# Kernel tuning notes

Hardware: AMD Instinct MI355X
Metric: run time of the kernel (lower is better)

The kernel has to match this reference:

```python
import jax, jax.numpy as jnp
from jax import lax
import numpy as np

EPS = 1e-3  # Keras BatchNormalization default epsilon

def cond_conv(x, experts, rw, rb):
    # x: [B,H,W,Cin]; experts: [E,kh,kw,Cin,Cout]
    pooled = jnp.mean(x, axis=(1, 2))                       # [B,Cin]
    route = jax.nn.sigmoid(pooled @ rw + rb)                # [B,E]
    kernels = jnp.einsum('be,ehwio->bhwio', route, experts) # per-example kernel
    def conv1(xi, ki):
        return lax.conv_general_dilated(
            xi[None], ki, window_strides=(1, 1), padding='SAME',
            dimension_numbers=('NHWC', 'HWIO', 'NHWC'))[0]
    return jax.vmap(conv1)(x, kernels)

def bn_inf(x, gamma, beta, mean, var):
    inv = gamma * lax.rsqrt(var + EPS)
    return x * inv + (beta - mean * inv)

def maxpool2(x):
    return lax.reduce_window(x, -jnp.inf, lax.max,
                             (1, 2, 2, 1), (1, 2, 2, 1), 'SAME')

def se_block(x, w1, w2):
    s = jnp.mean(x, axis=(1, 2))          # [B,C]
    s = jax.nn.relu(s @ w1)
    s = jax.nn.sigmoid(s @ w2)
    return x * s[:, None, None, :]

def setup_inputs() -> dict:
    key = jax.random.key(0)
    ks = jax.random.split(key, 12)
    d = {
        'x': jax.random.normal(ks[0], (64, 128, 128, 6), jnp.float32),
        'experts1': jax.random.normal(ks[1], (3, 3, 3, 6, 32), jnp.float32) * 0.1,
        'route1_w': jax.random.normal(ks[2], (6, 3), jnp.float32) * 0.1,
        'route1_b': jnp.zeros((3,), jnp.float32),
        'bn1_gamma': jnp.ones((32,), jnp.float32), 'bn1_beta': jnp.zeros((32,), jnp.float32),
        'bn1_mean': jnp.zeros((32,), jnp.float32), 'bn1_var': jnp.ones((32,), jnp.float32),
        'se1_w1': jax.random.normal(ks[3], (32, 2), jnp.float32) * 0.1,
        'se1_w2': jax.random.normal(ks[4], (2, 32), jnp.float32) * 0.1,
        'experts2': jax.random.normal(ks[5], (3, 3, 3, 32, 64), jnp.float32) * 0.05,
        'route2_w': jax.random.normal(ks[6], (32, 3), jnp.float32) * 0.1,
        'route2_b': jnp.zeros((3,), jnp.float32),
        'bn2_gamma': jnp.ones((64,), jnp.float32), 'bn2_beta': jnp.zeros((64,), jnp.float32),
        'bn2_mean': jnp.zeros((64,), jnp.float32), 'bn2_var': jnp.ones((64,), jnp.float32),
        'se2_w1': jax.random.normal(ks[7], (64, 4), jnp.float32) * 0.1,
        'se2_w2': jax.random.normal(ks[8], (4, 64), jnp.float32) * 0.1,
        'experts3': jax.random.normal(ks[9], (3, 3, 3, 64, 128), jnp.float32) * 0.05,
        'route3_w': jax.random.normal(ks[10], (64, 3), jnp.float32) * 0.1,
        'route3_b': jnp.zeros((3,), jnp.float32),
        'bn3_gamma': jnp.ones((128,), jnp.float32), 'bn3_beta': jnp.zeros((128,), jnp.float32),
        'bn3_mean': jnp.zeros((128,), jnp.float32), 'bn3_var': jnp.ones((128,), jnp.float32),
    }
    return d

def reference(x, experts1, route1_w, route1_b, bn1_gamma, bn1_beta, bn1_mean, bn1_var,
              se1_w1, se1_w2, experts2, route2_w, route2_b, bn2_gamma, bn2_beta,
              bn2_mean, bn2_var, se2_w1, se2_w2, experts3, route3_w, route3_b,
              bn3_gamma, bn3_beta, bn3_mean, bn3_var):
    h = cond_conv(x, experts1, route1_w, route1_b)
    h = jax.nn.relu(bn_inf(h, bn1_gamma, bn1_beta, bn1_mean, bn1_var))
    h = maxpool2(h)                       # [B,64,64,32]
    h = se_block(h, se1_w1, se1_w2)
    h = cond_conv(h, experts2, route2_w, route2_b)
    h = jax.nn.relu(bn_inf(h, bn2_gamma, bn2_beta, bn2_mean, bn2_var))
    h = maxpool2(h)                       # [B,32,32,64]
    h = se_block(h, se2_w1, se2_w2)
    h = cond_conv(h, experts3, route3_w, route3_b)
    h = bn_inf(h, bn3_gamma, bn3_beta, bn3_mean, bn3_var)
    return jnp.mean(h, axis=(1, 2))       # [B,128]
```

## Files before the change

kernel.cpp:

```cpp
#include <hip/hip_runtime.h>

#define EPSBN 1e-3f

typedef unsigned short ushort_t;
typedef __attribute__((ext_vector_type(8))) short bf8;
typedef __attribute__((ext_vector_type(4))) float f4;

__device__ __forceinline__ float sigmoidf_(float z) {
  return 1.0f / (1.0f + expf(-z));
}

__device__ __forceinline__ ushort_t f2bf(float x) {
  union { float f; unsigned u; } v; v.f = x;
  unsigned r = (v.u + 0x7fffu + ((v.u >> 16) & 1u)) >> 16;
  return (ushort_t)r;
}

__global__ void k_mean_x(const float* __restrict__ x, float* __restrict__ part) {
  const int b = blockIdx.x >> 2;
  const int q = blockIdx.x & 3;
  const int tid = threadIdx.x;
  float acc[6] = {0.f, 0.f, 0.f, 0.f, 0.f, 0.f};
  const float* xb = x + (size_t)b * 98304 + (size_t)q * 24576;
  for (int p = 0; p < 4; ++p) {
    const float* base = xb + (size_t)p * 6144 + (size_t)tid * 24;
#pragma unroll
    for (int k = 0; k < 6; ++k) {
      const float4 v = *(const float4*)(base + k * 4);
      acc[(4 * k + 0) % 6] += v.x;
      acc[(4 * k + 1) % 6] += v.y;
      acc[(4 * k + 2) % 6] += v.z;
      acc[(4 * k + 3) % 6] += v.w;
    }
  }
#pragma unroll
  for (int c = 0; c < 6; ++c)
    for (int off = 32; off > 0; off >>= 1) acc[c] += __shfl_down(acc[c], off, 64);
  __shared__ float red[4][6];
  const int lane = tid & 63, w = tid >> 6;
  if (lane == 0) {
#pragma unroll
    for (int c = 0; c < 6; ++c) red[w][c] = acc[c];
  }
  __syncthreads();
  if (tid < 6) {
    part[blockIdx.x * 6 + tid] = red[0][tid] + red[1][tid] + red[2][tid] + red[3][tid];
  }
}

__global__ __launch_bounds__(256)
void k_conv1(const float* __restrict__ x, const float* __restrict__ meanx_part,
             const float* __restrict__ experts1,
             const float* __restrict__ rw, const float* __restrict__ rbias,
             const float* __restrict__ gamma, const float* __restrict__ beta,
             const float* __restrict__ bnmean, const float* __restrict__ bnvar,
             ushort_t* __restrict__ p1b, float* __restrict__ part_m1) {
  const int bid = blockIdx.x;
  const int b = bid >> 3;
  const int tyi = (bid >> 1) & 3;
  const int txi = bid & 1;
  __shared__ __align__(16) ushort_t patch[34 * 68 * 8];
  __shared__ float route_s[3];
  __shared__ float mred[4][32];
  const int tid = threadIdx.x;
  const float* xb = x + (size_t)b * (128 * 128 * 6);

  if (tid < 3) {
    float z = rbias[tid];
    for (int c = 0; c < 6; ++c) {
      const float s = meanx_part[(b * 4 + 0) * 6 + c] + meanx_part[(b * 4 + 1) * 6 + c] +
                      meanx_part[(b * 4 + 2) * 6 + c] + meanx_part[(b * 4 + 3) * 6 + c];
      z += (s * (1.0f / 16384.0f)) * rw[c * 3 + tid];
    }
    route_s[tid] = sigmoidf_(z);
  }

  for (int v = tid; v < 34 * 68; v += 256) {
    const int ry = v / 68, p = v - ry * 68;
    const int gy = tyi * 32 - 1 + ry, gx = txi * 64 - 1 + p;
    uint4 u = make_uint4(0u, 0u, 0u, 0u);
    if (((unsigned)gy < 128u) && ((unsigned)gx < 128u)) {
      const float* s = xb + ((size_t)(gy * 128 + gx)) * 6;
      const float2 a0 = *(const float2*)s;
      const float2 a1 = *(const float2*)(s + 2);
      const float2 a2 = *(const float2*)(s + 4);
      u.x = (unsigned)f2bf(a0.x) | ((unsigned)f2bf(a0.y) << 16);
      u.y = (unsigned)f2bf(a1.x) | ((unsigned)f2bf(a1.y) << 16);
      u.z = (unsigned)f2bf(a2.x) | ((unsigned)f2bf(a2.y) << 16);
      u.w = 0u;
    }
    *(uint4*)(patch + (size_t)v * 8) = u;
  }
  __syncthreads();

  const int w = tid >> 6;
  const int lane = tid & 63;
  const int lx = lane & 15, lg = lane >> 4;

  const float r0 = route_s[0], r1 = route_s[1], r2 = route_s[2];
  const int co0 = lx, co1 = 16 + lx;
  const float inv0 = gamma[co0] * rsqrtf(bnvar[co0] + EPSBN);
  const float bias0 = beta[co0] - bnmean[co0] * inv0;
  const float inv1 = gamma[co1] * rsqrtf(bnvar[co1] + EPSBN);
  const float bias1 = beta[co1] - bnmean[co1] * inv1;

  bf8 Bf[3][2];
#pragma unroll
  for (int ky = 0; ky < 3; ++ky) {
#pragma unroll
    for (int nt = 0; nt < 2; ++nt) {
      const int co = nt * 16 + lx;
      const float inv = nt ? inv1 : inv0;
#pragma unroll
      for (int j = 0; j < 8; ++j) {
        float val = 0.f;
        if (j < 6 && lg < 3) {
          const int idx = ((ky * 3 + lg) * 6 + j) * 32 + co;
          val = (r0 * experts1[idx] + r1 * experts1[1728 + idx] +
                 r2 * experts1[3456 + idx]) * inv;
        }
        Bf[ky][nt][j] = (short)f2bf(val);
      }
    }
  }

  float msum0 = 0.f, msum1 = 0.f;

#pragma unroll
  for (int xt = 0; xt < 4; ++xt) {
    bf8 Af[10];
#pragma unroll
    for (int r = 0; r < 10; ++r)
      Af[r] = *(const bf8*)(patch + ((size_t)(w * 8 + r) * 68 + xt * 16 + lx + lg) * 8);
#pragma unroll
    for (int rp = 0; rp < 4; ++rp) {
      const int prow = tyi * 16 + w * 4 + rp;
      f4 acc0[2], acc1[2];
#pragma unroll
      for (int nt = 0; nt < 2; ++nt) {
        acc0[nt] = (f4){0.f, 0.f, 0.f, 0.f};
        acc1[nt] = (f4){0.f, 0.f, 0.f, 0.f};
      }
#pragma unroll
      for (int ky = 0; ky < 3; ++ky) {
#pragma unroll
        for (int nt = 0; nt < 2; ++nt) {
          acc0[nt] = __builtin_amdgcn_mfma_f32_16x16x32_bf16(Af[rp * 2 + ky], Bf[ky][nt], acc0[nt], 0, 0, 0);
          acc1[nt] = __builtin_amdgcn_mfma_f32_16x16x32_bf16(Af[rp * 2 + ky + 1], Bf[ky][nt], acc1[nt], 0, 0, 0);
        }
      }
#pragma unroll
      for (int nt = 0; nt < 2; ++nt) {
        const float bias = nt ? bias1 : bias0;
        const int co = nt * 16 + lx;
#pragma unroll
        for (int q = 0; q < 2; ++q) {
          const float m0 = fmaxf(acc0[nt][2 * q] + bias, 0.f);
          const float m1 = fmaxf(acc0[nt][2 * q + 1] + bias, 0.f);
          const float m2 = fmaxf(acc1[nt][2 * q] + bias, 0.f);
          const float m3 = fmaxf(acc1[nt][2 * q + 1] + bias, 0.f);
          const float mx = fmaxf(fmaxf(m0, m1), fmaxf(m2, m3));
          if (nt) msum1 += mx; else msum0 += mx;
          const int pcol = txi * 32 + xt * 8 + lg * 2 + q;
          p1b[(((size_t)b * 64 + prow) * 64 + pcol) * 32 + co] = f2bf(mx);
        }
      }
    }
  }

  msum0 += __shfl_xor(msum0, 16, 64);
  msum0 += __shfl_xor(msum0, 32, 64);
  msum1 += __shfl_xor(msum1, 16, 64);
  msum1 += __shfl_xor(msum1, 32, 64);
  if (lg == 0) {
    mred[w][lx] = msum0;
    mred[w][16 + lx] = msum1;
  }
  __syncthreads();
  if (tid < 32) {
    part_m1[(size_t)bid * 32 + tid] =
        mred[0][tid] + mred[1][tid] + mred[2][tid] + mred[3][tid];
  }
}

__global__ void k_buildk2(const float* __restrict__ part_m1,
                          const float* __restrict__ experts2,
                          const float* __restrict__ rw, const float* __restrict__ rb,
                          const float* __restrict__ w1, const float* __restrict__ w2,
                          const float* __restrict__ gamma, const float* __restrict__ var,
                          ushort_t* __restrict__ k2pb) {
  const int b = blockIdx.x / 3;
  const int seg = blockIdx.x - b * 3;
  const int tid = threadIdx.x;
  __shared__ float m1[32], h[2], s1[32], route[3];
  if (tid < 32) {
    float s = 0.f;
#pragma unroll
    for (int k = 0; k < 8; ++k) s += part_m1[(size_t)(b * 8 + k) * 32 + tid];
    m1[tid] = s * (1.0f / 4096.0f);
  }
  __syncthreads();
  if (tid < 2) {
    float z = 0.f;
    for (int c = 0; c < 32; ++c) z += m1[c] * w1[c * 2 + tid];
    h[tid] = fmaxf(z, 0.f);
  }
  __syncthreads();
  if (tid < 32) s1[tid] = sigmoidf_(h[0] * w2[tid] + h[1] * w2[32 + tid]);
  __syncthreads();
  if (tid < 3) {
    float z = rb[tid];
    for (int c = 0; c < 32; ++c) z += m1[c] * s1[c] * rw[c * 3 + tid];
    route[tid] = sigmoidf_(z);
  }
  __syncthreads();
  const float r0 = route[0], r1 = route[1], r2 = route[2];
  const int t_lo = seg * 6144, t_hi = t_lo + 6144;
  for (int t = t_lo + tid; t < t_hi; t += 256) {
    const int co = t & 63;
    const int ci = (t >> 6) & 31;
    const int tap = t >> 11;
    const float inv = gamma[co] * rsqrtf(var[co] + EPSBN);
    const float v = r0 * experts2[t] + r1 * experts2[18432 + t] + r2 * experts2[2 * 18432 + t];
    k2pb[(size_t)b * 18432 + ((size_t)tap * 64 + co) * 32 + ci] = f2bf(v * s1[ci] * inv);
  }
}

__global__ __launch_bounds__(256)
void k_conv2(const ushort_t* __restrict__ p1b, const ushort_t* __restrict__ k2pb,
             const float* __restrict__ gamma, const float* __restrict__ beta,
             const float* __restrict__ bnmean, const float* __restrict__ bnvar,
             float* __restrict__ part_s3) {
  const int bi = blockIdx.x;
  const int b = bi >> 5;
  const int tile = (bi >> 1) & 15;
  const int cog = bi & 1;
  const int ty = tile >> 2, tx = tile & 3;
  __shared__ __align__(16) short smem[24480];
  short* As = smem;
  short* Bs = smem + 12960;
  const int tid = threadIdx.x;

  const ushort_t* pb = p1b + (size_t)b * 131072;
  for (int v = tid; v < 1296; v += 256) {
    const int cell = v >> 2, part = v & 3;
    const int ly = cell / 18, lx2 = cell - ly * 18;
    const int gy = ty * 16 - 1 + ly, gx = tx * 16 - 1 + lx2;
    uint4 d = make_uint4(0u, 0u, 0u, 0u);
    if (((unsigned)gy < 64u) && ((unsigned)gx < 64u))
      d = *(const uint4*)(pb + (((size_t)gy << 6) + gx) * 32 + part * 8);
    *(uint4*)(As + (ly * 18 + lx2) * 40 + part * 8) = d;
  }
  for (int v = tid; v < 1152; v += 256) {
    const int r = v >> 2, part = v & 3;
    const int t = r >> 5, n = r & 31;
    const uint4 d = *(const uint4*)(k2pb + (size_t)b * 18432 +
                                    ((size_t)(t * 64 + cog * 32 + n)) * 32 + part * 8);
    *(uint4*)(Bs + r * 40 + part * 8) = d;
  }
  __syncthreads();

  const int w = tid >> 6;
  const int lane = tid & 63;
  const int lx = lane & 15, lg = lane >> 4;

  f4 acc[4][2];
#pragma unroll
  for (int mt = 0; mt < 4; ++mt)
#pragma unroll
    for (int nt = 0; nt < 2; ++nt)
      acc[mt][nt] = (f4){0.f, 0.f, 0.f, 0.f};

#pragma unroll
  for (int kx = 0; kx < 3; ++kx) {
    bf8 Af[6];
#pragma unroll
    for (int r = 0; r < 6; ++r)
      Af[r] = *(const bf8*)(As + ((4 * w + r) * 18 + lx + kx) * 40 + (lg << 3));
#pragma unroll
    for (int ky = 0; ky < 3; ++ky) {
      const int t = ky * 3 + kx;
      const bf8 Bf0 = *(const bf8*)(Bs + ((t << 5) + lx) * 40 + (lg << 3));
      const bf8 Bf1 = *(const bf8*)(Bs + ((t << 5) + 16 + lx) * 40 + (lg << 3));
#pragma unroll
      for (int mt = 0; mt < 4; ++mt) {
        acc[mt][0] = __builtin_amdgcn_mfma_f32_16x16x32_bf16(Af[ky + mt], Bf0, acc[mt][0], 0, 0, 0);
        acc[mt][1] = __builtin_amdgcn_mfma_f32_16x16x32_bf16(Af[ky + mt], Bf1, acc[mt][1], 0, 0, 0);
      }
    }
  }

  float inv[2], bias[2];
#pragma unroll
  for (int nt = 0; nt < 2; ++nt) {
    const int co = cog * 32 + nt * 16 + lx;
    inv[nt] = gamma[co] * rsqrtf(bnvar[co] + EPSBN);
    bias[nt] = beta[co] - bnmean[co] * inv[nt];
  }
  float agg[2][9];
#pragma unroll
  for (int nt = 0; nt < 2; ++nt)
#pragma unroll
    for (int a = 0; a < 9; ++a) agg[nt][a] = 0.f;

#pragma unroll
  for (int half = 0; half < 2; ++half) {
    const int prow = ty * 8 + 2 * w + half;
    const bool rT = (prow == 0), rB = (prow == 31);
#pragma unroll
    for (int q = 0; q < 2; ++q) {
      const int pcol = tx * 8 + 2 * lg + q;
      const bool cL = (pcol == 0), cR = (pcol == 31);
#pragma unroll
      for (int nt = 0; nt < 2; ++nt) {
        const float m0 = fmaxf(acc[2 * half][nt][2 * q] + bias[nt], 0.f);
        const float m1 = fmaxf(acc[2 * half][nt][2 * q + 1] + bias[nt], 0.f);
        const float m2 = fmaxf(acc[2 * half + 1][nt][2 * q] + bias[nt], 0.f);
        const float m3 = fmaxf(acc[2 * half + 1][nt][2 * q + 1] + bias[nt], 0.f);
        const float mx = fmaxf(fmaxf(m0, m1), fmaxf(m2, m3));
        agg[nt][0] += mx;
        if (rT) agg[nt][1] += mx;
        if (rB) agg[nt][2] += mx;
        if (cL) agg[nt][3] += mx;
        if (cR) agg[nt][4] += mx;
        if (rT && cL) agg[nt][5] += mx;
        if (rT && cR) agg[nt][6] += mx;
        if (rB && cL) agg[nt][7] += mx;
        if (rB && cR) agg[nt][8] += mx;
      }
    }
  }

#pragma unroll
  for (int nt = 0; nt < 2; ++nt)
#pragma unroll
    for (int a = 0; a < 9; ++a) {
      float v = agg[nt][a];
      v += __shfl_xor(v, 16, 64);
      v += __shfl_xor(v, 32, 64);
      agg[nt][a] = v;
    }
  __syncthreads();
  float* sred = (float*)smem;
  if (lg == 0) {
#pragma unroll
    for (int nt = 0; nt < 2; ++nt)
#pragma unroll
      for (int a = 0; a < 9; ++a)
        sred[((w * 2 + nt) * 16 + lx) * 9 + a] = agg[nt][a];
  }
  __syncthreads();
  for (int v = tid; v < 288; v += 256) {
    const int a = v >> 5;
    const int colocal = v & 31;
    const int nt = colocal >> 4, lxx = colocal & 15;
    float s = 0.f;
#pragma unroll
    for (int ww = 0; ww < 4; ++ww) s += sred[((ww * 2 + nt) * 16 + lxx) * 9 + a];
    part_s3[(size_t)bi * 288 + v] = s;
  }
}

__global__ __launch_bounds__(512)
void k_final(const float* __restrict__ part_s3, const float* __restrict__ experts3,
             const float* __restrict__ rw, const float* __restrict__ rb,
             const float* __restrict__ w1, const float* __restrict__ w2,
             const float* __restrict__ gamma, const float* __restrict__ beta,
             const float* __restrict__ bnmean, const float* __restrict__ bnvar,
             float* __restrict__ out) {
  const int b = blockIdx.x;
  const int tid = threadIdx.x;
  __shared__ float AG[9][64], Sp[9][64], m2[64], h[4], s2[64], route[3], redf[4][128];

  for (int v = tid; v < 576; v += 512) {
    const int a = v >> 6, ci = v & 63;
    const int cg = ci >> 5, colocal = ci & 31;
    float s = 0.f;
#pragma unroll
    for (int tile = 0; tile < 16; ++tile)
      s += part_s3[(size_t)((b * 16 + tile) * 2 + cg) * 288 + a * 32 + colocal];
    AG[a][ci] = s;
  }
  __syncthreads();
  if (tid < 64) m2[tid] = AG[0][tid] * (1.0f / 1024.0f);
  __syncthreads();
  if (tid < 4) {
    float z = 0.f;
    for (int c = 0; c < 64; ++c) z += m2[c] * w1[c * 4 + tid];
    h[tid] = fmaxf(z, 0.f);
  }
  __syncthreads();
  if (tid < 64) {
    float z = 0.f;
#pragma unroll
    for (int j = 0; j < 4; ++j) z += h[j] * w2[j * 64 + tid];
    s2[tid] = sigmoidf_(z);
  }
  __syncthreads();
  if (tid < 3) {
    float z = rb[tid];
    for (int c = 0; c < 64; ++c) z += m2[c] * s2[c] * rw[c * 3 + tid];
    route[tid] = sigmoidf_(z);
  }
  __syncthreads();
  for (int v = tid; v < 576; v += 512) {
    const int tap = v >> 6, ci = v & 63;
    const int ky = tap / 3, kx = tap - 3 * ky;
    const float T = AG[0][ci];
    const float A = (ky == 0) ? AG[2][ci] : ((ky == 2) ? AG[1][ci] : 0.f);
    const float B = (kx == 0) ? AG[4][ci] : ((kx == 2) ? AG[3][ci] : 0.f);
    float AB = 0.f;
    if (ky == 0 && kx == 0) AB = AG[8][ci];
    else if (ky == 0 && kx == 2) AB = AG[7][ci];
    else if (ky == 2 && kx == 0) AB = AG[6][ci];
    else if (ky == 2 && kx == 2) AB = AG[5][ci];
    Sp[tap][ci] = (T - A - B + AB) * s2[ci];
  }
  __syncthreads();

  const int co = tid & 127;
  const int quarter = tid >> 7;
  const int tap_lo = (quarter == 0) ? 0 : (2 * quarter + 1);
  const int tap_hi = tap_lo + ((quarter == 0) ? 3 : 2);
  float acc = 0.f;
#pragma unroll
  for (int e = 0; e < 3; ++e) {
    float m = 0.f;
    for (int tap = tap_lo; tap < tap_hi; ++tap) {
      const float* E = experts3 + ((size_t)(e * 9 + tap) * 64) * 128 + co;
#pragma unroll 16
      for (int ci = 0; ci < 64; ++ci) m = fmaf(E[(size_t)ci * 128], Sp[tap][ci], m);
    }
    acc += route[e] * m;
  }
  redf[quarter][co] = acc;
  __syncthreads();
  if (tid < 128) {
    const float total = redf[0][tid] + redf[1][tid] + redf[2][tid] + redf[3][tid];
    const float inv = gamma[tid] * rsqrtf(bnvar[tid] + EPSBN);
    out[(size_t)b * 128 + tid] = total * (1.0f / 1024.0f) * inv + (beta[tid] - bnmean[tid] * inv);
  }
}

extern "C" void kernel_launch(void* const* d_in, const int* in_sizes, int n_in,
                              void* d_out, int out_size, void* d_ws, size_t ws_size,
                              hipStream_t stream) {
  const float* x        = (const float*)d_in[0];
  const float* experts1 = (const float*)d_in[1];
  const float* rw1      = (const float*)d_in[2];
  const float* rb1      = (const float*)d_in[3];
  const float* g1  = (const float*)d_in[4];
  const float* be1 = (const float*)d_in[5];
  const float* mu1 = (const float*)d_in[6];
  const float* va1 = (const float*)d_in[7];
  const float* sw1a = (const float*)d_in[8];
  const float* sw1b = (const float*)d_in[9];
  const float* experts2 = (const float*)d_in[10];
  const float* rw2 = (const float*)d_in[11];
  const float* rb2 = (const float*)d_in[12];
  const float* g2  = (const float*)d_in[13];
  const float* be2 = (const float*)d_in[14];
  const float* mu2 = (const float*)d_in[15];
  const float* va2 = (const float*)d_in[16];
  const float* sw2a = (const float*)d_in[17];
  const float* sw2b = (const float*)d_in[18];
  const float* experts3 = (const float*)d_in[19];
  const float* rw3 = (const float*)d_in[20];
  const float* rb3 = (const float*)d_in[21];
  const float* g3  = (const float*)d_in[22];
  const float* be3 = (const float*)d_in[23];
  const float* mu3 = (const float*)d_in[24];
  const float* va3 = (const float*)d_in[25];
  float* out = (float*)d_out;
  float* ws = (float*)d_ws;

  float* meanx_part = ws;
  float* part_m1    = ws + 1536;
  ushort_t* k2pb    = (ushort_t*)(ws + 17920);
  float* part_s3    = ws + 607744;
  ushort_t* p1b     = (ushort_t*)(ws + 1197568);

  hipLaunchKernelGGL(k_mean_x, dim3(256), dim3(256), 0, stream, x, meanx_part);
  hipLaunchKernelGGL(k_conv1, dim3(512), dim3(256), 0, stream,
                     x, meanx_part, experts1, rw1, rb1, g1, be1, mu1, va1, p1b, part_m1);
  hipLaunchKernelGGL(k_buildk2, dim3(192), dim3(256), 0, stream,
                     part_m1, experts2, rw2, rb2, sw1a, sw1b, g2, va2, k2pb);
  hipLaunchKernelGGL(k_conv2, dim3(2048), dim3(256), 0, stream,
                     p1b, k2pb, g2, be2, mu2, va2, part_s3);
  hipLaunchKernelGGL(k_final, dim3(64), dim3(512), 0, stream,
                     part_s3, experts3, rw3, rb3, sw2a, sw2b, g3, be3, mu3, va3, out);
}
```

Before: 191.8 us.

## Pre-convert input to padded bf16, merge conv2 channel groups, fuse expert loop

The mean-reduction kernel now also writes the input as padded 8-channel bf16, so conv1's halo loads become single 16-byte reads without per-pixel conversion. conv2 has each block loop over both 32-channel output groups, reusing the loaded input patch and halving the grid. The final kernel computes all three expert sums in one pass over ci. The trade-off is an extra bf16 workspace write and read, and less parallelism in conv2.

After: 195.7 us. 2.1% more time.

```diff
diff --git a/kernel.cpp b/kernel.cpp
--- a/kernel.cpp
+++ b/kernel.cpp
@@ -16,40 +16,56 @@
   return (ushort_t)r;
 }
 
-__global__ void k_mean_x(const float* __restrict__ x, float* __restrict__ part) {
-  const int b = blockIdx.x >> 2;
-  const int q = blockIdx.x & 3;
+__global__ __launch_bounds__(256)
+void k_prep(const float* __restrict__ x, float* __restrict__ part,
+            ushort_t* __restrict__ xb16) {
+  const int bid = blockIdx.x;
   const int tid = threadIdx.x;
+  __shared__ __align__(16) float raw[3072];
+  __shared__ float red[4][6];
   float acc[6] = {0.f, 0.f, 0.f, 0.f, 0.f, 0.f};
-  const float* xb = x + (size_t)b * 98304 + (size_t)q * 24576;
-  for (int p = 0; p < 4; ++p) {
-    const float* base = xb + (size_t)p * 6144 + (size_t)tid * 24;
-#pragma unroll
-    for (int k = 0; k < 6; ++k) {
-      const float4 v = *(const float4*)(base + k * 4);
-      acc[(4 * k + 0) % 6] += v.x;
-      acc[(4 * k + 1) % 6] += v.y;
-      acc[(4 * k + 2) % 6] += v.z;
-      acc[(4 * k + 3) % 6] += v.w;
-    }
-  }
+  const size_t pixbase = (size_t)(bid >> 3) * 16384 + (size_t)(bid & 7) * 2048;
+  const float* xq = x + pixbase * 6;
+  ushort_t* oq = xb16 + pixbase * 8;
+  for (int ph = 0; ph < 4; ++ph) {
+    const float4* src = (const float4*)(xq + (size_t)ph * 3072);
+#pragma unroll
+    for (int i = 0; i < 3; ++i)
+      *(float4*)(raw + (i * 256 + tid) * 4) = src[i * 256 + tid];
+    __syncthreads();
+#pragma unroll
+    for (int h = 0; h < 2; ++h) {
+      const int pix = h * 256 + tid;
+      const float* r = raw + pix * 6;
+      const float2 p01 = *(const float2*)(r);
+      const float2 p23 = *(const float2*)(r + 2);
+      const float2 p45 = *(const float2*)(r + 4);
+      acc[0] += p01.x; acc[1] += p01.y; acc[2] += p23.x;
+      acc[3] += p23.y; acc[4] += p45.x; acc[5] += p45.y;
+      uint4 u;
+      u.x = (unsigned)f2bf(p01.x) | ((unsigned)f2bf(p01.y) << 16);
+      u.y = (unsigned)f2bf(p23.x) | ((unsigned)f2bf(p23.y) << 16);
+      u.z = (unsigned)f2bf(p45.x) | ((unsigned)f2bf(p45.y) << 16);
+      u.w = 0u;
+      *(uint4*)(oq + ((size_t)ph * 512 + pix) * 8) = u;
+    }
+    __syncthreads();
+  }
+  const int lane = tid & 63, w = tid >> 6;
 #pragma unroll
   for (int c = 0; c < 6; ++c)
     for (int off = 32; off > 0; off >>= 1) acc[c] += __shfl_down(acc[c], off, 64);
-  __shared__ float red[4][6];
-  const int lane = tid & 63, w = tid >> 6;
   if (lane == 0) {
 #pragma unroll
     for (int c = 0; c < 6; ++c) red[w][c] = acc[c];
   }
   __syncthreads();
-  if (tid < 6) {
-    part[blockIdx.x * 6 + tid] = red[0][tid] + red[1][tid] + red[2][tid] + red[3][tid];
-  }
+  if (tid < 6)
+    part[bid * 6 + tid] = red[0][tid] + red[1][tid] + red[2][tid] + red[3][tid];
 }
 
 __global__ __launch_bounds__(256)
-void k_conv1(const float* __restrict__ x, const float* __restrict__ meanx_part,
+void k_conv1(const ushort_t* __restrict__ xb16, const float* __restrict__ meanx_part,
              const float* __restrict__ experts1,
              const float* __restrict__ rw, const float* __restrict__ rbias,
              const float* __restrict__ gamma, const float* __restrict__ beta,
@@ -63,13 +79,14 @@
   __shared__ float route_s[3];
   __shared__ float mred[4][32];
   const int tid = threadIdx.x;
-  const float* xb = x + (size_t)b * (128 * 128 * 6);
+  const ushort_t* xb = xb16 + (size_t)b * 131072;
 
   if (tid < 3) {
     float z = rbias[tid];
     for (int c = 0; c < 6; ++c) {
-      const float s = meanx_part[(b * 4 + 0) * 6 + c] + meanx_part[(b * 4 + 1) * 6 + c] +
-                      meanx_part[(b * 4 + 2) * 6 + c] + meanx_part[(b * 4 + 3) * 6 + c];
+      float s = 0.f;
+#pragma unroll
+      for (int k = 0; k < 8; ++k) s += meanx_part[(b * 8 + k) * 6 + c];
       z += (s * (1.0f / 16384.0f)) * rw[c * 3 + tid];
     }
     route_s[tid] = sigmoidf_(z);
@@ -79,16 +96,8 @@
     const int ry = v / 68, p = v - ry * 68;
     const int gy = tyi * 32 - 1 + ry, gx = txi * 64 - 1 + p;
     uint4 u = make_uint4(0u, 0u, 0u, 0u);
-    if (((unsigned)gy < 128u) && ((unsigned)gx < 128u)) {
-      const float* s = xb + ((size_t)(gy * 128 + gx)) * 6;
-      const float2 a0 = *(const float2*)s;
-      const float2 a1 = *(const float2*)(s + 2);
-      const float2 a2 = *(const float2*)(s + 4);
-      u.x = (unsigned)f2bf(a0.x) | ((unsigned)f2bf(a0.y) << 16);
-      u.y = (unsigned)f2bf(a1.x) | ((unsigned)f2bf(a1.y) << 16);
-      u.z = (unsigned)f2bf(a2.x) | ((unsigned)f2bf(a2.y) << 16);
-      u.w = 0u;
-    }
+    if (((unsigned)gy < 128u) && ((unsigned)gx < 128u))
+      u = *(const uint4*)(xb + ((size_t)(gy * 128 + gx)) * 8);
     *(uint4*)(patch + (size_t)v * 8) = u;
   }
   __syncthreads();
@@ -232,11 +241,10 @@
              const float* __restrict__ bnmean, const float* __restrict__ bnvar,
              float* __restrict__ part_s3) {
   const int bi = blockIdx.x;
-  const int b = bi >> 5;
-  const int tile = (bi >> 1) & 15;
-  const int cog = bi & 1;
+  const int b = bi >> 4;
+  const int tile = bi & 15;
   const int ty = tile >> 2, tx = tile & 3;
-  __shared__ __align__(16) short smem[24480];
+  __shared__ __align__(16) short smem[12960 + 11520];
   short* As = smem;
   short* Bs = smem + 12960;
   const int tid = threadIdx.x;
@@ -251,113 +259,118 @@
       d = *(const uint4*)(pb + (((size_t)gy << 6) + gx) * 32 + part * 8);
     *(uint4*)(As + (ly * 18 + lx2) * 40 + part * 8) = d;
   }
-  for (int v = tid; v < 1152; v += 256) {
-    const int r = v >> 2, part = v & 3;
-    const int t = r >> 5, n = r & 31;
-    const uint4 d = *(const uint4*)(k2pb + (size_t)b * 18432 +
-                                    ((size_t)(t * 64 + cog * 32 + n)) * 32 + part * 8);
-    *(uint4*)(Bs + r * 40 + part * 8) = d;
-  }
-  __syncthreads();
 
   const int w = tid >> 6;
   const int lane = tid & 63;
   const int lx = lane & 15, lg = lane >> 4;
 
-  f4 acc[4][2];
-#pragma unroll
-  for (int mt = 0; mt < 4; ++mt)
-#pragma unroll
-    for (int nt = 0; nt < 2; ++nt)
-      acc[mt][nt] = (f4){0.f, 0.f, 0.f, 0.f};
-
-#pragma unroll
-  for (int kx = 0; kx < 3; ++kx) {
-    bf8 Af[6];
-#pragma unroll
-    for (int r = 0; r < 6; ++r)
-      Af[r] = *(const bf8*)(As + ((4 * w + r) * 18 + lx + kx) * 40 + (lg << 3));
-#pragma unroll
-    for (int ky = 0; ky < 3; ++ky) {
-      const int t = ky * 3 + kx;
-      const bf8 Bf0 = *(const bf8*)(Bs + ((t << 5) + lx) * 40 + (lg << 3));
-      const bf8 Bf1 = *(const bf8*)(Bs + ((t << 5) + 16 + lx) * 40 + (lg << 3));
-#pragma unroll
-      for (int mt = 0; mt < 4; ++mt) {
-        acc[mt][0] = __builtin_amdgcn_mfma_f32_16x16x32_bf16(Af[ky + mt], Bf0, acc[mt][0], 0, 0, 0);
-        acc[mt][1] = __builtin_amdgcn_mfma_f32_16x16x32_bf16(Af[ky + mt], Bf1, acc[mt][1], 0, 0, 0);
+  float agg[4][9];
+#pragma unroll
+  for (int g = 0; g < 4; ++g)
+#pragma unroll
+    for (int a = 0; a < 9; ++a) agg[g][a] = 0.f;
+
+  for (int cg = 0; cg < 2; ++cg) {
+    if (cg) __syncthreads();
+    for (int v = tid; v < 1152; v += 256) {
+      const int r = v >> 2, part = v & 3;
+      const int t = r >> 5, n = r & 31;
+      const uint4 d = *(const uint4*)(k2pb + (size_t)b * 18432 +
+                                      ((size_t)(t * 64 + cg * 32 + n)) * 32 + part * 8);
+      *(uint4*)(Bs + r * 40 + part * 8) = d;
+    }
+    __syncthreads();
+
+    f4 acc[4][2];
+#pragma unroll
+    for (int mt = 0; mt < 4; ++mt) {
+      acc[mt][0] = (f4){0.f, 0.f, 0.f, 0.f};
+      acc[mt][1] = (f4){0.f, 0.f, 0.f, 0.f};
+    }
+
+#pragma unroll
+    for (int kx = 0; kx < 3; ++kx) {
+      bf8 Af[6];
+#pragma unroll
+      for (int r = 0; r < 6; ++r)
+        Af[r] = *(const bf8*)(As + ((4 * w + r) * 18 + lx + kx) * 40 + (lg << 3));
+#pragma unroll
+      for (int ky = 0; ky < 3; ++ky) {
+        const int t = ky * 3 + kx;
+        const bf8 Bf0 = *(const bf8*)(Bs + ((t << 5) + lx) * 40 + (lg << 3));
+        const bf8 Bf1 = *(const bf8*)(Bs + ((t << 5) + 16 + lx) * 40 + (lg << 3));
+#pragma unroll
+        for (int mt = 0; mt < 4; ++mt) {
+          acc[mt][0] = __builtin_amdgcn_mfma_f32_16x16x32_bf16(Af[ky + mt], Bf0, acc[mt][0], 0, 0, 0);
+          acc[mt][1] = __builtin_amdgcn_mfma_f32_16x16x32_bf16(Af[ky + mt], Bf1, acc[mt][1], 0, 0, 0);
+        }
       }
     }
-  }
-
-  float inv[2], bias[2];
-#pragma unroll
-  for (int nt = 0; nt < 2; ++nt) {
-    const int co = cog * 32 + nt * 16 + lx;
-    inv[nt] = gamma[co] * rsqrtf(bnvar[co] + EPSBN);
-    bias[nt] = beta[co] - bnmean[co] * inv[nt];
-  }
-  float agg[2][9];
-#pragma unroll
-  for (int nt = 0; nt < 2; ++nt)
-#pragma unroll
-    for (int a = 0; a < 9; ++a) agg[nt][a] = 0.f;
-
-#pragma unroll
-  for (int half = 0; half < 2; ++half) {
-    const int prow = ty * 8 + 2 * w + half;
-    const bool rT = (prow == 0), rB = (prow == 31);
-#pragma unroll
-    for (int q = 0; q < 2; ++q) {
-      const int pcol = tx * 8 + 2 * lg + q;
-      const bool cL = (pcol == 0), cR = (pcol == 31);
-#pragma unroll
-      for (int nt = 0; nt < 2; ++nt) {
-        const float m0 = fmaxf(acc[2 * half][nt][2 * q] + bias[nt], 0.f);
-        const float m1 = fmaxf(acc[2 * half][nt][2 * q + 1] + bias[nt], 0.f);
-        const float m2 = fmaxf(acc[2 * half + 1][nt][2 * q] + bias[nt], 0.f);
-        const float m3 = fmaxf(acc[2 * half + 1][nt][2 * q + 1] + bias[nt], 0.f);
-        const float mx = fmaxf(fmaxf(m0, m1), fmaxf(m2, m3));
-        agg[nt][0] += mx;
-        if (rT) agg[nt][1] += mx;
-        if (rB) agg[nt][2] += mx;
-        if (cL) agg[nt][3] += mx;
-        if (cR) agg[nt][4] += mx;
-        if (rT && cL) agg[nt][5] += mx;
-        if (rT && cR) agg[nt][6] += mx;
-        if (rB && cL) agg[nt][7] += mx;
-        if (rB && cR) agg[nt][8] += mx;
+
+    float inv[2], bias[2];
+#pragma unroll
+    for (int nt = 0; nt < 2; ++nt) {
+      const int co = cg * 32 + nt * 16 + lx;
+      inv[nt] = gamma[co] * rsqrtf(bnvar[co] + EPSBN);
+      bias[nt] = beta[co] - bnmean[co] * inv[nt];
+    }
+#pragma unroll
+    for (int half = 0; half < 2; ++half) {
+      const int prow = ty * 8 + 2 * w + half;
+      const bool rT = (prow == 0), rB = (prow == 31);
+#pragma unroll
+      for (int q = 0; q < 2; ++q) {
+        const int pcol = tx * 8 + 2 * lg + q;
+        const bool cL = (pcol == 0), cR = (pcol == 31);
+#pragma unroll
+        for (int nt = 0; nt < 2; ++nt) {
+          const float m0 = fmaxf(acc[2 * half][nt][2 * q] + bias[nt], 0.f);
+          const float m1 = fmaxf(acc[2 * half][nt][2 * q + 1] + bias[nt], 0.f);
+          const float m2 = fmaxf(acc[2 * half + 1][nt][2 * q] + bias[nt], 0.f);
+          const float m3 = fmaxf(acc[2 * half + 1][nt][2 * q + 1] + bias[nt], 0.f);
+          const float mx = fmaxf(fmaxf(m0, m1), fmaxf(m2, m3));
+          float* ag = agg[cg * 2 + nt];
+          ag[0] += mx;
+          if (rT) ag[1] += mx;
+          if (rB) ag[2] += mx;
+          if (cL) ag[3] += mx;
+          if (cR) ag[4] += mx;
+          if (rT && cL) ag[5] += mx;
+          if (rT && cR) ag[6] += mx;
+          if (rB && cL) ag[7] += mx;
+          if (rB && cR) ag[8] += mx;
+        }
       }
     }
   }
 
 #pragma unroll
-  for (int nt = 0; nt < 2; ++nt)
+  for (int g = 0; g < 4; ++g)
 #pragma unroll
     for (int a = 0; a < 9; ++a) {
-      float v = agg[nt][a];
-      v += __shfl_xor(v, 16, 64);
-      v += __shfl_xor(v, 32, 64);
-      agg[nt][a] = v;
+      float vv = agg[g][a];
+      vv += __shfl_xor(vv, 16, 64);
+      vv += __shfl_xor(vv, 32, 64);
+      agg[g][a] = vv;
     }
   __syncthreads();
   float* sred = (float*)smem;
   if (lg == 0) {
 #pragma unroll
-    for (int nt = 0; nt < 2; ++nt)
+    for (int g = 0; g < 4; ++g)
 #pragma unroll
       for (int a = 0; a < 9; ++a)
-        sred[((w * 2 + nt) * 16 + lx) * 9 + a] = agg[nt][a];
-  }
-  __syncthreads();
-  for (int v = tid; v < 288; v += 256) {
-    const int a = v >> 5;
-    const int colocal = v & 31;
-    const int nt = colocal >> 4, lxx = colocal & 15;
+        sred[((w * 4 + g) * 16 + lx) * 9 + a] = agg[g][a];
+  }
+  __syncthreads();
+  for (int v = tid; v < 576; v += 256) {
+    const int a = v >> 6;
+    const int co = v & 63;
+    const int g = co >> 4, lxx = co & 15;
     float s = 0.f;
 #pragma unroll
-    for (int ww = 0; ww < 4; ++ww) s += sred[((ww * 2 + nt) * 16 + lxx) * 9 + a];
-    part_s3[(size_t)bi * 288 + v] = s;
+    for (int ww = 0; ww < 4; ++ww) s += sred[((ww * 4 + g) * 16 + lxx) * 9 + a];
+    part_s3[(size_t)bi * 576 + v] = s;
   }
 }
 
@@ -374,11 +387,10 @@
 
   for (int v = tid; v < 576; v += 512) {
     const int a = v >> 6, ci = v & 63;
-    const int cg = ci >> 5, colocal = ci & 31;
     float s = 0.f;
 #pragma unroll
     for (int tile = 0; tile < 16; ++tile)
-      s += part_s3[(size_t)((b * 16 + tile) * 2 + cg) * 288 + a * 32 + colocal];
+      s += part_s3[(size_t)(b * 16 + tile) * 576 + a * 64 + ci];
     AG[a][ci] = s;
   }
   __syncthreads();
@@ -422,18 +434,20 @@
   const int quarter = tid >> 7;
   const int tap_lo = (quarter == 0) ? 0 : (2 * quarter + 1);
   const int tap_hi = tap_lo + ((quarter == 0) ? 3 : 2);
-  float acc = 0.f;
-#pragma unroll
-  for (int e = 0; e < 3; ++e) {
-    float m = 0.f;
-    for (int tap = tap_lo; tap < tap_hi; ++tap) {
-      const float* E = experts3 + ((size_t)(e * 9 + tap) * 64) * 128 + co;
+  float me0 = 0.f, me1 = 0.f, me2 = 0.f;
+  for (int tap = tap_lo; tap < tap_hi; ++tap) {
+    const float* E0 = experts3 + ((size_t)tap * 64) * 128 + co;
+    const float* E1 = E0 + (size_t)9 * 64 * 128;
+    const float* E2 = E1 + (size_t)9 * 64 * 128;
 #pragma unroll 16
-      for (int ci = 0; ci < 64; ++ci) m = fmaf(E[(size_t)ci * 128], Sp[tap][ci], m);
-    }
-    acc += route[e] * m;
-  }
-  redf[quarter][co] = acc;
+    for (int ci = 0; ci < 64; ++ci) {
+      const float s = Sp[tap][ci];
+      me0 = fmaf(E0[(size_t)ci * 128], s, me0);
+      me1 = fmaf(E1[(size_t)ci * 128], s, me1);
+      me2 = fmaf(E2[(size_t)ci * 128], s, me2);
+    }
+  }
+  redf[quarter][co] = route[0] * me0 + route[1] * me1 + route[2] * me2;
   __syncthreads();
   if (tid < 128) {
     const float total = redf[0][tid] + redf[1][tid] + redf[2][tid] + redf[3][tid];
@@ -475,17 +489,18 @@
   float* ws = (float*)d_ws;
 
   float* meanx_part = ws;
-  float* part_m1    = ws + 1536;
-  ushort_t* k2pb    = (ushort_t*)(ws + 17920);
-  float* part_s3    = ws + 607744;
-  ushort_t* p1b     = (ushort_t*)(ws + 1197568);
-
-  hipLaunchKernelGGL(k_mean_x, dim3(256), dim3(256), 0, stream, x, meanx_part);
+  float* part_m1    = ws + 3072;
+  ushort_t* k2pb    = (ushort_t*)(ws + 19456);
+  float* part_s3    = ws + 609280;
+  ushort_t* p1b     = (ushort_t*)(ws + 1199104);
+  ushort_t* xb16    = (ushort_t*)(ws + 5393408);
+
+  hipLaunchKernelGGL(k_prep, dim3(512), dim3(256), 0, stream, x, meanx_part, xb16);
   hipLaunchKernelGGL(k_conv1, dim3(512), dim3(256), 0, stream,
-                     x, meanx_part, experts1, rw1, rb1, g1, be1, mu1, va1, p1b, part_m1);
+                     xb16, meanx_part, experts1, rw1, rb1, g1, be1, mu1, va1, p1b, part_m1);
   hipLaunchKernelGGL(k_buildk2, dim3(192), dim3(256), 0, stream,
                      part_m1, experts2, rw2, rb2, sw1a, sw1b, g2, va2, k2pb);
-  hipLaunchKernelGGL(k_conv2, dim3(2048), dim3(256), 0, stream,
+  hipLaunchKernelGGL(k_conv2, dim3(1024), dim3(256), 0, stream,
                      p1b, k2pb, g2, be2, mu2, va2, part_s3);
   hipLaunchKernelGGL(k_final, dim3(64), dim3(512), 0, stream,
                      part_s3, experts3, rw3, rb3, sw2a, sw2b, g3, be3, mu3, va3, out);
```
